# Kernel optimization log

Hardware: AMD Instinct MI355X
Metric: run time of the kernel (lower is better)

Reference implementation:

```python
import jax, jax.numpy as jnp
import numpy as np

# Constants from the torch module
S_DECAY = 0.95    # sentence_decay
P_DECAY = 0.99    # paragraph_decay
D_DECAY = 0.999   # document_decay
ALPHA = 0.1       # delta_update alpha for sentence/paragraph
DOC_ALPHA = 0.05  # delta_update alpha for document
BETA = 1.0
PARA_GROUP = 5    # sentences per paragraph
EPS = 1e-12       # F.normalize eps


def _normalize(x):
    # matches torch.nn.functional.normalize(x, dim=-1)
    return x / jnp.maximum(jnp.linalg.norm(x, axis=-1, keepdims=True), EPS)


def _delta_step(M, kn, v, alpha, beta):
    # M: [H, dk, dv]; kn: [dk] (already L2-normalized); v: [dv]
    # M_new = M @ (I - alpha * kn kn^T) + beta * kn v^T   (erase matrix is symmetric,
    # so the einsum 'hkv,hkj->hjv' form equals this rank-1 update -- no dk x dk matrix needed)
    kTM = jnp.einsum('k,hkv->hv', kn, M)                       # [H, dv]
    return M - alpha * kn[None, :, None] * kTM[:, None, :] \
             + beta * (kn[:, None] * v[None, :])[None, :, :]


def _scan_updates(M0, K, V, decay, alpha, beta):
    # Streaming delta-rule: per step, decay then erase/write.
    def step(M, kv):
        k, v = kv
        M = M * decay
        M = _delta_step(M, _normalize(k), v, alpha, beta)
        return M, None
    M, _ = jax.lax.scan(step, M0, (K, V))
    return M


def setup_inputs() -> dict:
    key = jax.random.key(0)
    ks = jax.random.split(key, 7)
    T, d_emb, d_k, d_v, H = 1000, 768, 256, 256, 8
    emb = jax.random.normal(ks[0], (T, d_emb), dtype=jnp.float32)
    q = jax.random.normal(ks[1], (d_k,), dtype=jnp.float32)
    W_k = jax.random.normal(ks[2], (d_emb, d_k), dtype=jnp.float32) * 0.02
    b_k = jax.random.normal(ks[3], (d_k,), dtype=jnp.float32) * 0.02
    W_v = jax.random.normal(ks[4], (d_emb, d_v), dtype=jnp.float32) * 0.02
    b_v = jax.random.normal(ks[5], (d_v,), dtype=jnp.float32) * 0.02
    M_sent0 = jnp.zeros((H, d_k, d_v), dtype=jnp.float32)
    M_para0 = jnp.zeros((H, d_k, d_v), dtype=jnp.float32)
    M_doc0 = jnp.zeros((H, d_k, d_v), dtype=jnp.float32)
    return {"emb": emb, "q": q, "W_k": W_k, "b_k": b_k, "W_v": W_v, "b_v": b_v,
            "M_sent0": M_sent0, "M_para0": M_para0, "M_doc0": M_doc0}


def reference(emb, q, W_k, b_k, W_v, b_v, M_sent0, M_para0, M_doc0):
    T, d_emb = emb.shape
    # Level 1: sentence memory -- one delta update per sentence embedding
    K = emb @ W_k + b_k            # [T, dk]
    V = emb @ W_v + b_v            # [T, dv]
    M_sent = _scan_updates(M_sent0, K, V, S_DECAY, ALPHA, BETA)
    # Level 2: paragraph memory -- mean of each group of 5 sentence embeddings
    para_emb = emb.reshape(T // PARA_GROUP, PARA_GROUP, d_emb).mean(axis=1)
    PK = para_emb @ W_k + b_k
    PV = para_emb @ W_v + b_v
    M_para = _scan_updates(M_para0, PK, PV, P_DECAY, ALPHA, BETA)
    # Level 3: document memory -- single update from paragraph-memory statistics
    doc_k = M_para.mean(axis=0).mean(axis=-1)   # [dk]
    doc_v = M_para.mean(axis=0).mean(axis=0)    # [dv]
    M_doc = M_doc0 * D_DECAY
    M_doc = _delta_step(M_doc, _normalize(doc_k), doc_v, DOC_ALPHA, BETA)
    # recall(q, level='all')
    qn = _normalize(q)
    def recall(M):
        return jnp.einsum('hkv,k->hv', M, qn).mean(axis=0)   # [dv]
    return 0.2 * recall(M_sent) + 0.3 * recall(M_para) + 0.5 * recall(M_doc)
```

## Files before the change

### kernel.cpp

```cpp
#include <hip/hip_runtime.h>
#include <hip/hip_bf16.h>

#define ALPHA   0.1f
#define S_DECAY 0.95f
#define P_DECAY 0.99f
#define D_EMB   768
#define DK      256

template<int ctrl, int row_mask>
__device__ __forceinline__ float dpp_add(float x) {
    int y = __builtin_amdgcn_update_dpp(0, __float_as_int(x), ctrl, row_mask, 0xF, true);
    return x + __int_as_float(y);
}

template<int N>
__device__ __forceinline__ void wave_allred_arr(float (&x)[N]) {
#pragma unroll
    for (int n = 0; n < N; ++n) x[n] = dpp_add<0xB1,  0xF>(x[n]);
#pragma unroll
    for (int n = 0; n < N; ++n) x[n] = dpp_add<0x4E,  0xF>(x[n]);
#pragma unroll
    for (int n = 0; n < N; ++n) x[n] = dpp_add<0x141, 0xF>(x[n]);
#pragma unroll
    for (int n = 0; n < N; ++n) x[n] = dpp_add<0x140, 0xF>(x[n]);
#pragma unroll
    for (int n = 0; n < N; ++n) x[n] = dpp_add<0x142, 0xA>(x[n]);
#pragma unroll
    for (int n = 0; n < N; ++n) x[n] = dpp_add<0x143, 0xC>(x[n]);
#pragma unroll
    for (int n = 0; n < N; ++n)
        x[n] = __int_as_float(__builtin_amdgcn_readlane(__float_as_int(x[n]), 63));
}

__device__ __forceinline__ float dot4v(const float4& a, const float4& b) {
    float t0 = a.x * b.x; t0 = fmaf(a.y, b.y, t0);
    float t1 = a.z * b.z; t1 = fmaf(a.w, b.w, t1);
    return t0 + t1;
}

__global__ __launch_bounds__(256) void prep_kernel(
    const float* __restrict__ emb,
    const float* __restrict__ Wk, const float* __restrict__ bk,
    const float* __restrict__ Wv, const float* __restrict__ bv,
    float* __restrict__ K, float* __restrict__ V, float* __restrict__ USrev,
    float* __restrict__ out, int T)
{
    const int tid = threadIdx.x;
    const int bid = blockIdx.x;
    const int NBLK = (T / 4) * 2;
    if (bid >= NBLK) {
        const int PADS = ((T + 63) / 64) * 64;
        for (int i = tid; i < (PADS - T) * DK; i += 256) USrev[(size_t)T * DK + i] = 0.f;
        out[tid] = 0.f;
        return;
    }
    const int mat = bid & 1;
    const int r0  = (bid >> 1) * 4;

    __shared__ float se[4][D_EMB];
    __shared__ float s_red[4][4];

    const float4* emb4 = reinterpret_cast<const float4*>(emb);
#pragma unroll
    for (int r = 0; r < 4; ++r) {
        if (tid < D_EMB / 4)
            reinterpret_cast<float4*>(se[r])[tid] = emb4[(size_t)(r0 + r) * (D_EMB / 4) + tid];
    }
    __syncthreads();

    const float* Wp = mat ? Wv : Wk;
    const float* bp = mat ? bv : bk;
    const int j = tid;

    float a0 = 0.f, a1 = 0.f, a2 = 0.f, a3 = 0.f;
    float c0 = Wp[j],        c1 = Wp[j + DK],     c2 = Wp[j + 2*DK], c3 = Wp[j + 3*DK];
    float p0 = Wp[j + 4*DK], p1 = Wp[j + 5*DK],   p2 = Wp[j + 6*DK], p3 = Wp[j + 7*DK];

    for (int d = 0; d < D_EMB; d += 4) {
        int dn = d + 8; if (dn >= D_EMB) dn = 0;
        const float* wn = Wp + (size_t)dn * DK + j;
        float n0 = wn[0], n1 = wn[DK], n2 = wn[2*DK], n3 = wn[3*DK];

        float4 e0 = *reinterpret_cast<const float4*>(&se[0][d]);
        float4 e1 = *reinterpret_cast<const float4*>(&se[1][d]);
        float4 e2 = *reinterpret_cast<const float4*>(&se[2][d]);
        float4 e3 = *reinterpret_cast<const float4*>(&se[3][d]);

        a0 = fmaf(e0.x, c0, a0); a0 = fmaf(e0.y, c1, a0);
        a0 = fmaf(e0.z, c2, a0); a0 = fmaf(e0.w, c3, a0);
        a1 = fmaf(e1.x, c0, a1); a1 = fmaf(e1.y, c1, a1);
        a1 = fmaf(e1.z, c2, a1); a1 = fmaf(e1.w, c3, a1);
        a2 = fmaf(e2.x, c0, a2); a2 = fmaf(e2.y, c1, a2);
        a2 = fmaf(e2.z, c2, a2); a2 = fmaf(e2.w, c3, a2);
        a3 = fmaf(e3.x, c0, a3); a3 = fmaf(e3.y, c1, a3);
        a3 = fmaf(e3.z, c2, a3); a3 = fmaf(e3.w, c3, a3);

        c0 = p0; c1 = p1; c2 = p2; c3 = p3;
        p0 = n0; p1 = n1; p2 = n2; p3 = n3;
    }

    float bj = bp[j];
    float o0 = a0 + bj, o1 = a1 + bj, o2 = a2 + bj, o3 = a3 + bj;
    float* dst = mat ? V : K;
    dst[(size_t)(r0 + 0) * DK + j] = o0;
    dst[(size_t)(r0 + 1) * DK + j] = o1;
    dst[(size_t)(r0 + 2) * DK + j] = o2;
    dst[(size_t)(r0 + 3) * DK + j] = o3;

    if (mat == 0) {
        const int wave = tid >> 6, l = tid & 63;
        float red[4] = { o0*o0, o1*o1, o2*o2, o3*o3 };
        wave_allred_arr(red);
        if (l == 0) {
            s_red[wave][0] = red[0]; s_red[wave][1] = red[1];
            s_red[wave][2] = red[2]; s_red[wave][3] = red[3];
        }
        __syncthreads();
        float t0 = s_red[0][0] + s_red[1][0] + s_red[2][0] + s_red[3][0];
        float t1 = s_red[0][1] + s_red[1][1] + s_red[2][1] + s_red[3][1];
        float t2 = s_red[0][2] + s_red[1][2] + s_red[2][2] + s_red[3][2];
        float t3 = s_red[0][3] + s_red[1][3] + s_red[2][3] + s_red[3][3];
        USrev[(size_t)(T - 1 - (r0 + 0)) * DK + j] = o0 * (1.0f / fmaxf(sqrtf(t0), 1e-12f));
        USrev[(size_t)(T - 1 - (r0 + 1)) * DK + j] = o1 * (1.0f / fmaxf(sqrtf(t1), 1e-12f));
        USrev[(size_t)(T - 1 - (r0 + 2)) * DK + j] = o2 * (1.0f / fmaxf(sqrtf(t2), 1e-12f));
        USrev[(size_t)(T - 1 - (r0 + 3)) * DK + j] = o3 * (1.0f / fmaxf(sqrtf(t3), 1e-12f));
    }
}

__global__ __launch_bounds__(256) void graminv_kernel(
    const float* __restrict__ K, const float* __restrict__ V,
    const float* __restrict__ USrev,
    float* __restrict__ UPrev, float* __restrict__ UPfwd,
    float* __restrict__ PV, float* __restrict__ SVv,
    float* __restrict__ AinvT, float* __restrict__ Wall,
    float* __restrict__ F1, float* __restrict__ biasF,
    int P, int NCS, int NCP)
{
    __shared__ float sU[64 * 257];
    __shared__ float sA[64 * 65];
    __shared__ float sX[64 * 65];
    __shared__ float s_sv[64];
    __shared__ float s_pd[64];
    __shared__ float4 s_f1[4];
    __shared__ float4 s_f1w[4][64];
    const int tid = threadIdx.x, wv = tid >> 6, l = tid & 63;
    const int bid = blockIdx.x;
    int type, m;
    if (bid < NCS)            { type = 0; m = bid; }
    else if (bid < NCS + NCP) { type = 1; m = bid - NCS; }
    else                      { type = 2; m = bid - NCS - NCP; }

    if (tid < 64) s_pd[tid] = powf(P_DECAY, (float)tid);

    float4 f1p = make_float4(0.f, 0.f, 0.f, 0.f);

    if (type == 0) {
        const float4* U4 = reinterpret_cast<const float4*>(USrev) + (size_t)m * 4096;
        for (int idx = tid; idx < 4096; idx += 256) {
            float4 t = U4[idx];
            int row = idx >> 6, c4 = (idx & 63) << 2;
            float* b = &sU[row * 257 + c4];
            b[0] = t.x; b[1] = t.y; b[2] = t.z; b[3] = t.w;
        }
    } else if (type == 1) {
        const float4* K4 = reinterpret_cast<const float4*>(K);
        for (int ii = 0; ii < 16; ++ii) {
            int i = wv * 16 + ii;
            int p = P - 1 - (64 * m + i);
            float4 u = make_float4(0.f, 0.f, 0.f, 0.f);
            if (p >= 0) {
                float4 pk = make_float4(0.f, 0.f, 0.f, 0.f);
#pragma unroll
                for (int s = 0; s < 5; ++s) {
                    float4 k4 = K4[(size_t)(5 * p + s) * 64 + l];
                    pk.x += k4.x; pk.y += k4.y; pk.z += k4.z; pk.w += k4.w;
                }
                pk.x *= 0.2f; pk.y *= 0.2f; pk.z *= 0.2f; pk.w *= 0.2f;
                float red[1] = { dot4v(pk, pk) };
                wave_allred_arr(red);
                float inv = 1.0f / fmaxf(sqrtf(red[0]), 1e-12f);
                u = make_float4(pk.x * inv, pk.y * inv, pk.z * inv, pk.w * inv);
            }
            float* b = &sU[i * 257 + 4 * l];
            b[0] = u.x; b[1] = u.y; b[2] = u.z; b[3] = u.w;
            reinterpret_cast<float4*>(UPrev)[(size_t)(64 * m + i) * 64 + l] = u;
        }
    } else {
        const float4* K4 = reinterpret_cast<const float4*>(K);
        const float4* V4 = reinterpret_cast<const float4*>(V);
        for (int ii = 0; ii < 16; ++ii) {
            int i = wv * 16 + ii;
            int p = 64 * m + i;
            float4 u = make_float4(0.f, 0.f, 0.f, 0.f);
            float sv = 0.f;
            if (p < P) {
                float4 pk = make_float4(0.f, 0.f, 0.f, 0.f);
                float4 pv = make_float4(0.f, 0.f, 0.f, 0.f);
#pragma unroll
                for (int s = 0; s < 5; ++s) {
                    float4 k4 = K4[(size_t)(5 * p + s) * 64 + l];
                    float4 v4 = V4[(size_t)(5 * p + s) * 64 + l];
                    pk.x += k4.x; pk.y += k4.y; pk.z += k4.z; pk.w += k4.w;
                    pv.x += v4.x; pv.y += v4.y; pv.z += v4.z; pv.w += v4.w;
                }
                pk.x *= 0.2f; pk.y *= 0.2f; pk.z *= 0.2f; pk.w *= 0.2f;
                pv.x *= 0.2f; pv.y *= 0.2f; pv.z *= 0.2f; pv.w *= 0.2f;
                reinterpret_cast<float4*>(PV)[(size_t)p * 64 + l] = pv;
                float red[2] = { dot4v(pk, pk), pv.x + pv.y + pv.z + pv.w };
                wave_allred_arr(red);
                float inv = 1.0f / fmaxf(sqrtf(red[0]), 1e-12f);
                u = make_float4(pk.x * inv, pk.y * inv, pk.z * inv, pk.w * inv);
                sv = red[1];
            }
            float* b = &sU[i * 257 + 4 * l];
            b[0] = u.x; b[1] = u.y; b[2] = u.z; b[3] = u.w;
            reinterpret_cast<float4*>(UPfwd)[(size_t)(64 * m + i) * 64 + l] = u;
            if (l == 0) { s_sv[i] = sv; SVv[64 * m + i] = sv; }
            float f = powf(P_DECAY, (float)(63 - i)) * sv;
            f1p.x = fmaf(f, u.x, f1p.x); f1p.y = fmaf(f, u.y, f1p.y);
            f1p.z = fmaf(f, u.z, f1p.z); f1p.w = fmaf(f, u.w, f1p.w);
        }
        s_f1w[wv][l] = f1p;
    }
    __syncthreads();

    if (type == 2 && wv == 0) {
        float4 a = s_f1w[0][l], b = s_f1w[1][l], c = s_f1w[2][l], d = s_f1w[3][l];
        float4 tot = make_float4(a.x+b.x+c.x+d.x, a.y+b.y+c.y+d.y,
                                 a.z+b.z+c.z+d.z, a.w+b.w+c.w+d.w);
        reinterpret_cast<float4*>(F1)[(size_t)m * 64 + l] = tot;
    }

    const int tr = tid & 15, tcg = tid >> 4;
    const int i0 = tr * 4, j0 = tcg * 4;
    {
        float g00=0,g01=0,g02=0,g03=0, g10=0,g11=0,g12=0,g13=0;
        float g20=0,g21=0,g22=0,g23=0, g30=0,g31=0,g32=0,g33=0;
        for (int k = 0; k < 256; ++k) {
            float aa0 = sU[(i0    ) * 257 + k];
            float aa1 = sU[(i0 + 1) * 257 + k];
            float aa2 = sU[(i0 + 2) * 257 + k];
            float aa3 = sU[(i0 + 3) * 257 + k];
            float bb0 = sU[(j0    ) * 257 + k];
            float bb1 = sU[(j0 + 1) * 257 + k];
            float bb2 = sU[(j0 + 2) * 257 + k];
            float bb3 = sU[(j0 + 3) * 257 + k];
            g00 = fmaf(aa0, bb0, g00); g01 = fmaf(aa0, bb1, g01);
            g02 = fmaf(aa0, bb2, g02); g03 = fmaf(aa0, bb3, g03);
            g10 = fmaf(aa1, bb0, g10); g11 = fmaf(aa1, bb1, g11);
            g12 = fmaf(aa1, bb2, g12); g13 = fmaf(aa1, bb3, g13);
            g20 = fmaf(aa2, bb0, g20); g21 = fmaf(aa2, bb1, g21);
            g22 = fmaf(aa2, bb2, g22); g23 = fmaf(aa2, bb3, g23);
            g30 = fmaf(aa3, bb0, g30); g31 = fmaf(aa3, bb1, g31);
            g32 = fmaf(aa3, bb2, g32); g33 = fmaf(aa3, bb3, g33);
        }
        float gt[4][4] = { {g00,g01,g02,g03}, {g10,g11,g12,g13},
                           {g20,g21,g22,g23}, {g30,g31,g32,g33} };
#pragma unroll
        for (int r = 0; r < 4; ++r)
#pragma unroll
            for (int c = 0; c < 4; ++c) {
                int gi = i0 + r, gj = j0 + c;
                float val = 0.f;
                if (gj < gi) {
                    val = ALPHA * gt[r][c];
                    if (type == 2) val *= s_pd[gi - gj];
                }
                sA[gi * 65 + gj] = val;
            }
    }
    __syncthreads();

    if (type == 2 && wv == 0) {
        float dotb = 0.f;
#pragma unroll
        for (int jj = 0; jj < 64; ++jj)
            dotb = fmaf(sA[l * 65 + jj], s_sv[jj], dotb);
        biasF[m * 64 + l] = dotb * (1.0f / ALPHA);
    }

    {
        const int base = wv * 16;
        float x[16];
#pragma unroll
        for (int r = 0; r < 16; ++r) x[r] = (base + r == l) ? 1.f : 0.f;
        for (int s = 0; s < 4; ++s) {
            if (wv == s) {
#pragma unroll
                for (int i = 1; i < 16; ++i)
#pragma unroll
                    for (int jj = 0; jj < 16; ++jj)
                        if (jj < i)
                            x[i] = fmaf(-sA[(base + i) * 65 + (base + jj)], x[jj], x[i]);
#pragma unroll
                for (int r = 0; r < 16; ++r) sX[(base + r) * 65 + l] = x[r];
            }
            __syncthreads();
            if (wv > s) {
#pragma unroll
                for (int i = 0; i < 16; ++i) {
                    float xi = sX[(s * 16 + i) * 65 + l];
#pragma unroll
                    for (int r = 0; r < 16; ++r)
                        x[r] = fmaf(-sA[(base + r) * 65 + (s * 16 + i)], xi, x[r]);
                }
            }
        }
    }
    __syncthreads();

    if (type != 2) {
        float* dstA = AinvT + (size_t)bid * 4096;
        for (int idx = tid; idx < 4096; idx += 256) {
            int jcol = idx >> 6, irow = idx & 63;
            dstA[idx] = sX[irow * 65 + jcol];
        }
    }

    {
        const int c0 = tcg * 16;
        float wacc[4][16];
#pragma unroll
        for (int r = 0; r < 4; ++r)
#pragma unroll
            for (int c = 0; c < 16; ++c) wacc[r][c] = 0.f;
        for (int i = 0; i < 64; ++i) {
            float x0 = sX[i * 65 + i0    ];
            float x1 = sX[i * 65 + i0 + 1];
            float x2 = sX[i * 65 + i0 + 2];
            float x3 = sX[i * 65 + i0 + 3];
            if (type == 2) {
                float f = s_pd[63 - i];
                x0 *= f; x1 *= f; x2 *= f; x3 *= f;
            }
#pragma unroll
            for (int c = 0; c < 16; ++c) {
                float u = sU[i * 257 + c0 + c];
                wacc[0][c] = fmaf(x0, u, wacc[0][c]);
                wacc[1][c] = fmaf(x1, u, wacc[1][c]);
                wacc[2][c] = fmaf(x2, u, wacc[2][c]);
                wacc[3][c] = fmaf(x3, u, wacc[3][c]);
            }
        }
        float* dstW = Wall + (size_t)bid * 16384;
#pragma unroll
        for (int r = 0; r < 4; ++r) {
#pragma unroll
            for (int c4 = 0; c4 < 4; ++c4) {
                float4 t = make_float4(wacc[r][c4*4], wacc[r][c4*4+1],
                                       wacc[r][c4*4+2], wacc[r][c4*4+3]);
                reinterpret_cast<float4*>(dstW)[((i0 + r) * 256 + c0 + c4*4) >> 2] = t;
            }
        }
    }
}

__global__ __launch_bounds__(512) void solve_kernel(
    const float* __restrict__ USrev, const float* __restrict__ UPrev,
    const float* __restrict__ UPfwd, const float* __restrict__ Wall,
    const float* __restrict__ F1, const float* __restrict__ biasF,
    const float* __restrict__ q,
    float* __restrict__ BS, float* __restrict__ BPB1, float* __restrict__ BPB2,
    float* __restrict__ gscal, int NCS, int NCP)
{
    __shared__ float4 s_part[2][8][64], s_part2[2][8][64];
    __shared__ float s_powd[65];
    const int tid = threadIdx.x, wave = tid >> 6, l = tid & 63;
    const int wb = wave * 8;
    if (tid <= 64) s_powd[tid] = powf(P_DECAY, (float)tid);

    float4 q4 = reinterpret_cast<const float4*>(q)[l];
    float qs[1] = { dot4v(q4, q4) };
    wave_allred_arr(qs);
    float qinv = 1.0f / fmaxf(sqrtf(qs[0]), 1e-12f);
    float4 qn = make_float4(q4.x * qinv, q4.y * qinv, q4.z * qinv, q4.w * qinv);
    __syncthreads();

    const float4* W4 = reinterpret_cast<const float4*>(Wall);

    if (blockIdx.x == 0) {
        float4 w1 = qn;
        const float4* U4 = reinterpret_cast<const float4*>(USrev);
        float4 curU[8];
#pragma unroll
        for (int r = 0; r < 8; ++r) curU[r] = U4[(size_t)(wb + r) * 64 + l];
        for (int m = 0; m < NCS; ++m) {
            float4 curW[8];
#pragma unroll
            for (int r = 0; r < 8; ++r)
                curW[r] = W4[(size_t)m * 4096 + (size_t)(wb + r) * 64 + l];
            float4 nxtU[8];
            if (m + 1 < NCS) {
#pragma unroll
                for (int r = 0; r < 8; ++r)
                    nxtU[r] = U4[(size_t)(m + 1) * 4096 + (size_t)(wb + r) * 64 + l];
            }
            float d[8];
#pragma unroll
            for (int r = 0; r < 8; ++r) d[r] = dot4v(curU[r], w1);
            wave_allred_arr(d);
            if (l == 0) {
#pragma unroll
                for (int r = 0; r < 8; ++r) BS[m * 64 + wb + r] = d[r];
            }
            float4 part = make_float4(0.f, 0.f, 0.f, 0.f);
#pragma unroll
            for (int r = 0; r < 8; ++r) {
                part.x = fmaf(d[r], curW[r].x, part.x);
                part.y = fmaf(d[r], curW[r].y, part.y);
                part.z = fmaf(d[r], curW[r].z, part.z);
                part.w = fmaf(d[r], curW[r].w, part.w);
            }
            s_part[m & 1][wave][l] = part;
            __syncthreads();
            float4 s = make_float4(0.f, 0.f, 0.f, 0.f);
#pragma unroll
            for (int w = 0; w < 8; ++w) {
                float4 p = s_part[m & 1][w][l];
                s.x += p.x; s.y += p.y; s.z += p.z; s.w += p.w;
            }
            w1.x = fmaf(-ALPHA, s.x, w1.x); w1.y = fmaf(-ALPHA, s.y, w1.y);
            w1.z = fmaf(-ALPHA, s.z, w1.z); w1.w = fmaf(-ALPHA, s.w, w1.w);
            if (m + 1 < NCS) {
#pragma unroll
                for (int r = 0; r < 8; ++r) curU[r] = nxtU[r];
            }
        }
    } else {
        {
            float4 w1 = qn;
            float4 w2 = make_float4(1.f, 1.f, 1.f, 1.f);
            const float4* U4 = reinterpret_cast<const float4*>(UPrev);
            float4 curU[8];
#pragma unroll
            for (int r = 0; r < 8; ++r) curU[r] = U4[(size_t)(wb + r) * 64 + l];
            for (int m = 0; m < NCP; ++m) {
                float4 curW[8];
#pragma unroll
                for (int r = 0; r < 8; ++r)
                    curW[r] = W4[(size_t)(NCS + m) * 4096 + (size_t)(wb + r) * 64 + l];
                float4 nxtU[8];
                if (m + 1 < NCP) {
#pragma unroll
                    for (int r = 0; r < 8; ++r)
                        nxtU[r] = U4[(size_t)(m + 1) * 4096 + (size_t)(wb + r) * 64 + l];
                }
                float d[16];
#pragma unroll
                for (int r = 0; r < 8; ++r) {
                    d[r]     = dot4v(curU[r], w1);
                    d[8 + r] = dot4v(curU[r], w2);
                }
                wave_allred_arr(d);
                if (l == 0) {
#pragma unroll
                    for (int r = 0; r < 8; ++r) {
                        BPB1[m * 64 + wb + r] = d[r];
                        BPB2[m * 64 + wb + r] = d[8 + r];
                    }
                }
                float4 p1 = make_float4(0.f,0.f,0.f,0.f), p2 = make_float4(0.f,0.f,0.f,0.f);
#pragma unroll
                for (int r = 0; r < 8; ++r) {
                    p1.x = fmaf(d[r], curW[r].x, p1.x);   p1.y = fmaf(d[r], curW[r].y, p1.y);
                    p1.z = fmaf(d[r], curW[r].z, p1.z);   p1.w = fmaf(d[r], curW[r].w, p1.w);
                    p2.x = fmaf(d[8+r], curW[r].x, p2.x); p2.y = fmaf(d[8+r], curW[r].y, p2.y);
                    p2.z = fmaf(d[8+r], curW[r].z, p2.z); p2.w = fmaf(d[8+r], curW[r].w, p2.w);
                }
                s_part[m & 1][wave][l] = p1; s_part2[m & 1][wave][l] = p2;
                __syncthreads();
                float4 s1 = make_float4(0.f,0.f,0.f,0.f), s2 = make_float4(0.f,0.f,0.f,0.f);
#pragma unroll
                for (int w = 0; w < 8; ++w) {
                    float4 a = s_part[m & 1][w][l];  float4 b = s_part2[m & 1][w][l];
                    s1.x += a.x; s1.y += a.y; s1.z += a.z; s1.w += a.w;
                    s2.x += b.x; s2.y += b.y; s2.z += b.z; s2.w += b.w;
                }
                w1.x = fmaf(-ALPHA, s1.x, w1.x); w1.y = fmaf(-ALPHA, s1.y, w1.y);
                w1.z = fmaf(-ALPHA, s1.z, w1.z); w1.w = fmaf(-ALPHA, s1.w, w1.w);
                w2.x = fmaf(-ALPHA, s2.x, w2.x); w2.y = fmaf(-ALPHA, s2.y, w2.y);
                w2.z = fmaf(-ALPHA, s2.z, w2.z); w2.w = fmaf(-ALPHA, s2.w, w2.w);
                if (m + 1 < NCP) {
#pragma unroll
                    for (int r = 0; r < 8; ++r) curU[r] = nxtU[r];
                }
            }
        }
        __syncthreads();
        float4 y = make_float4(0.f, 0.f, 0.f, 0.f);
        {
            const float4* U4 = reinterpret_cast<const float4*>(UPfwd);
            float4 curU[8];
#pragma unroll
            for (int r = 0; r < 8; ++r) curU[r] = U4[(size_t)(wb + r) * 64 + l];
            for (int m = 0; m < NCP; ++m) {
                float4 curW[8];
#pragma unroll
                for (int r = 0; r < 8; ++r)
                    curW[r] = W4[(size_t)(NCS + NCP + m) * 4096 + (size_t)(wb + r) * 64 + l];
                float biasr[8];
#pragma unroll
                for (int r = 0; r < 8; ++r) biasr[r] = biasF[m * 64 + wb + r];
                float4 f1 = reinterpret_cast<const float4*>(F1)[(size_t)m * 64 + l];
                float4 nxtU[8];
                if (m + 1 < NCP) {
#pragma unroll
                    for (int r = 0; r < 8; ++r)
                        nxtU[r] = U4[(size_t)(m + 1) * 4096 + (size_t)(wb + r) * 64 + l];
                }
                float d[8];
#pragma unroll
                for (int r = 0; r < 8; ++r) d[r] = dot4v(curU[r], y);
                wave_allred_arr(d);
#pragma unroll
                for (int r = 0; r < 8; ++r)
                    d[r] = fmaf(s_powd[wb + r + 1], d[r], biasr[r]);
                float4 part = make_float4(0.f, 0.f, 0.f, 0.f);
#pragma unroll
                for (int r = 0; r < 8; ++r) {
                    part.x = fmaf(d[r], curW[r].x, part.x);
                    part.y = fmaf(d[r], curW[r].y, part.y);
                    part.z = fmaf(d[r], curW[r].z, part.z);
                    part.w = fmaf(d[r], curW[r].w, part.w);
                }
                s_part[m & 1][wave][l] = part;
                __syncthreads();
                float4 s = make_float4(0.f, 0.f, 0.f, 0.f);
#pragma unroll
                for (int w = 0; w < 8; ++w) {
                    float4 p = s_part[m & 1][w][l];
                    s.x += p.x; s.y += p.y; s.z += p.z; s.w += p.w;
                }
                float d64 = s_powd[64];
                y.x = fmaf(d64, y.x, fmaf(-ALPHA, s.x, f1.x));
                y.y = fmaf(d64, y.y, fmaf(-ALPHA, s.y, f1.y));
                y.z = fmaf(d64, y.z, fmaf(-ALPHA, s.z, f1.z));
                y.w = fmaf(d64, y.w, fmaf(-ALPHA, s.w, f1.w));
                if (m + 1 < NCP) {
#pragma unroll
                    for (int r = 0; r < 8; ++r) curU[r] = nxtU[r];
                }
            }
        }
        float fin[2] = { dot4v(y, y), dot4v(qn, y) };
        wave_allred_arr(fin);
        if (tid == 0) gscal[0] = fin[1] / fmaxf(sqrtf(fin[0]), 2.56e-10f);
    }
}

__global__ __launch_bounds__(256) void accum_kernel(
    const float* __restrict__ V, const float* __restrict__ PV,
    const float* __restrict__ AinvT,
    const float* __restrict__ BS, const float* __restrict__ BPB1,
    const float* __restrict__ BPB2, const float* __restrict__ gscal,
    float* __restrict__ out, int T, int P, int NCS, int NCP)
{
    __shared__ float s_b[64], s_cp[4][64], wc[64];
    const int b = blockIdx.x, t = threadIdx.x;
    const float* src; const float* B; int i0, realN, chunk; float decay;
    if (b < NCS)            { src = V;  B = BS;   i0 = b * 64;               realN = T; decay = S_DECAY; chunk = b; }
    else if (b < NCS + NCP) { src = PV; B = BPB1; i0 = (b - NCS) * 64;       realN = P; decay = P_DECAY; chunk = b; }
    else                    { src = PV; B = BPB2; i0 = (b - NCS - NCP) * 64; realN = P; decay = P_DECAY; chunk = b - NCP; }
    if (t < 64) s_b[t] = B[(i0 & ~63) + t - i0 + i0];
    if (t < 64) s_b[t] = B[((b < NCS) ? b : (b < NCS + NCP ? b - NCS : b - NCS - NCP)) * 64 + t];
    __syncthreads();
    {
        const int part = t >> 6, k = t & 63;
        const float* Xc = AinvT + (size_t)chunk * 4096;
        float cp = 0.f;
#pragma unroll
        for (int jj = 0; jj < 16; ++jj) {
            int j = part * 16 + jj;
            cp = fmaf(Xc[j * 64 + k], s_b[j], cp);
        }
        s_cp[part][k] = cp;
    }
    __syncthreads();
    if (t < 64) {
        float c = s_cp[0][t] + s_cp[1][t] + s_cp[2][t] + s_cp[3][t];
        wc[t] = powf(decay, (float)(i0 + t)) * c;
    }
    __syncthreads();
    const int k = t;
    float acc = 0.f;
    for (int ii = 0; ii < 64; ++ii) {
        int i = i0 + ii;
        if (i < realN)
            acc = fmaf(wc[ii], src[(size_t)(realN - 1 - i) * DK + k], acc);
    }
    float wlev;
    if (b < NCS)            wlev = 0.2f;
    else if (b < NCS + NCP) wlev = 0.3f;
    else                    wlev = (0.5f / 256.0f) * gscal[0];
    atomicAdd(&out[k], wlev * acc);
}

extern "C" void kernel_launch(void* const* d_in, const int* in_sizes, int n_in,
                              void* d_out, int out_size, void* d_ws, size_t ws_size,
                              hipStream_t stream) {
    const float* emb = (const float*)d_in[0];
    const float* q   = (const float*)d_in[1];
    const float* Wk  = (const float*)d_in[2];
    const float* bk  = (const float*)d_in[3];
    const float* Wv  = (const float*)d_in[4];
    const float* bv  = (const float*)d_in[5];

    const int T = in_sizes[0] / D_EMB;
    const int P = T / 5;
    const int NCS  = (T + 63) / 64;
    const int NCP  = (P + 63) / 64;
    const int PADS = NCS * 64;
    const int PADP = NCP * 64;
    const int NCH  = NCS + 2 * NCP;

    float* ws    = (float*)d_ws;
    float* K     = ws;
    float* V     = K     + (size_t)T * DK;
    float* PV    = V     + (size_t)T * DK;
    float* USrev = PV    + (size_t)PADP * DK;
    float* UPrev = USrev + (size_t)PADS * DK;
    float* UPfwd = UPrev + (size_t)PADP * DK;
    float* SVv   = UPfwd + (size_t)PADP * DK;
    float* AinvT = SVv   + PADP;
    float* Wall  = AinvT + (size_t)NCH * 4096;
    float* F1    = Wall  + (size_t)NCH * 16384;
    float* biasF = F1    + (size_t)NCP * 256;
    float* BS    = biasF + PADP;
    float* BPB1  = BS    + PADS;
    float* BPB2  = BPB1  + PADP;
    float* gscal = BPB2  + PADP;

    prep_kernel<<<(T / 4) * 2 + 1, 256, 0, stream>>>(emb, Wk, bk, Wv, bv,
                                                     K, V, USrev, (float*)d_out, T);
    graminv_kernel<<<NCH, 256, 0, stream>>>(K, V, USrev, UPrev, UPfwd,
                                            PV, SVv, AinvT, Wall, F1, biasF, P, NCS, NCP);
    solve_kernel<<<2, 512, 0, stream>>>(USrev, UPrev, UPfwd, Wall, F1, biasF, q,
                                        BS, BPB1, BPB2, gscal, NCS, NCP);
    accum_kernel<<<NCH, 256, 0, stream>>>(V, PV, AinvT, BS, BPB1, BPB2, gscal,
                                          (float*)d_out, T, P, NCS, NCP);
}
```

Baseline: 198.4 us.

## Drop precomputed W matrices; apply inverse-then-U factored inside solve loop

The graminv kernel no longer builds and stores the per-chunk W = X·U products (64x256 per chunk) and only writes the transposed inverse. The sequential solve kernel instead applies X to the projected vector via a small cross-wave reduction, then broadcasts coefficients with readlane and multiplies by U, which it already loads. The Gram computation also uses float4 shared-memory reads with a padded stride and skips the upper-triangle tiles. This removes a large global write and read of W at the cost of an extra barrier and reduction per step in the latency-bound serial solve loop.

```diff
diff --git a/kernel.cpp b/kernel.cpp
--- a/kernel.cpp
+++ b/kernel.cpp
@@ -36,6 +36,10 @@
     float t0 = a.x * b.x; t0 = fmaf(a.y, b.y, t0);
     float t1 = a.z * b.z; t1 = fmaf(a.w, b.w, t1);
     return t0 + t1;
+}
+
+__device__ __forceinline__ float rl(float x, int lane) {
+    return __int_as_float(__builtin_amdgcn_readlane(__float_as_int(x), lane));
 }
 
 __global__ __launch_bounds__(256) void prep_kernel(
@@ -127,21 +131,20 @@
     }
 }
 
+#define SU_STRIDE 260
 __global__ __launch_bounds__(256) void graminv_kernel(
     const float* __restrict__ K, const float* __restrict__ V,
     const float* __restrict__ USrev,
     float* __restrict__ UPrev, float* __restrict__ UPfwd,
     float* __restrict__ PV, float* __restrict__ SVv,
-    float* __restrict__ AinvT, float* __restrict__ Wall,
-    float* __restrict__ F1, float* __restrict__ biasF,
+    float* __restrict__ AinvT, float* __restrict__ F1, float* __restrict__ biasF,
     int P, int NCS, int NCP)
 {
-    __shared__ float sU[64 * 257];
+    __shared__ float sU[64 * SU_STRIDE];
     __shared__ float sA[64 * 65];
     __shared__ float sX[64 * 65];
     __shared__ float s_sv[64];
     __shared__ float s_pd[64];
-    __shared__ float4 s_f1[4];
     __shared__ float4 s_f1w[4][64];
     const int tid = threadIdx.x, wv = tid >> 6, l = tid & 63;
     const int bid = blockIdx.x;
@@ -159,8 +162,7 @@
         for (int idx = tid; idx < 4096; idx += 256) {
             float4 t = U4[idx];
             int row = idx >> 6, c4 = (idx & 63) << 2;
-            float* b = &sU[row * 257 + c4];
-            b[0] = t.x; b[1] = t.y; b[2] = t.z; b[3] = t.w;
+            *reinterpret_cast<float4*>(&sU[row * SU_STRIDE + c4]) = t;
         }
     } else if (type == 1) {
         const float4* K4 = reinterpret_cast<const float4*>(K);
@@ -181,8 +183,7 @@
                 float inv = 1.0f / fmaxf(sqrtf(red[0]), 1e-12f);
                 u = make_float4(pk.x * inv, pk.y * inv, pk.z * inv, pk.w * inv);
             }
-            float* b = &sU[i * 257 + 4 * l];
-            b[0] = u.x; b[1] = u.y; b[2] = u.z; b[3] = u.w;
+            *reinterpret_cast<float4*>(&sU[i * SU_STRIDE + 4 * l]) = u;
             reinterpret_cast<float4*>(UPrev)[(size_t)(64 * m + i) * 64 + l] = u;
         }
     } else {
@@ -212,8 +213,7 @@
                 u = make_float4(pk.x * inv, pk.y * inv, pk.z * inv, pk.w * inv);
                 sv = red[1];
             }
-            float* b = &sU[i * 257 + 4 * l];
-            b[0] = u.x; b[1] = u.y; b[2] = u.z; b[3] = u.w;
+            *reinterpret_cast<float4*>(&sU[i * SU_STRIDE + 4 * l]) = u;
             reinterpret_cast<float4*>(UPfwd)[(size_t)(64 * m + i) * 64 + l] = u;
             if (l == 0) { s_sv[i] = sv; SVv[64 * m + i] = sv; }
             float f = powf(P_DECAY, (float)(63 - i)) * sv;
@@ -233,29 +233,30 @@
 
     const int tr = tid & 15, tcg = tid >> 4;
     const int i0 = tr * 4, j0 = tcg * 4;
-    {
-        float g00=0,g01=0,g02=0,g03=0, g10=0,g11=0,g12=0,g13=0;
-        float g20=0,g21=0,g22=0,g23=0, g30=0,g31=0,g32=0,g33=0;
-        for (int k = 0; k < 256; ++k) {
-            float aa0 = sU[(i0    ) * 257 + k];
-            float aa1 = sU[(i0 + 1) * 257 + k];
-            float aa2 = sU[(i0 + 2) * 257 + k];
-            float aa3 = sU[(i0 + 3) * 257 + k];
-            float bb0 = sU[(j0    ) * 257 + k];
-            float bb1 = sU[(j0 + 1) * 257 + k];
-            float bb2 = sU[(j0 + 2) * 257 + k];
-            float bb3 = sU[(j0 + 3) * 257 + k];
-            g00 = fmaf(aa0, bb0, g00); g01 = fmaf(aa0, bb1, g01);
-            g02 = fmaf(aa0, bb2, g02); g03 = fmaf(aa0, bb3, g03);
-            g10 = fmaf(aa1, bb0, g10); g11 = fmaf(aa1, bb1, g11);
-            g12 = fmaf(aa1, bb2, g12); g13 = fmaf(aa1, bb3, g13);
-            g20 = fmaf(aa2, bb0, g20); g21 = fmaf(aa2, bb1, g21);
-            g22 = fmaf(aa2, bb2, g22); g23 = fmaf(aa2, bb3, g23);
-            g30 = fmaf(aa3, bb0, g30); g31 = fmaf(aa3, bb1, g31);
-            g32 = fmaf(aa3, bb2, g32); g33 = fmaf(aa3, bb3, g33);
-        }
-        float gt[4][4] = { {g00,g01,g02,g03}, {g10,g11,g12,g13},
-                           {g20,g21,g22,g23}, {g30,g31,g32,g33} };
+    if (tcg <= tr) {
+        float g[4][4];
+#pragma unroll
+        for (int r = 0; r < 4; ++r)
+#pragma unroll
+            for (int c = 0; c < 4; ++c) g[r][c] = 0.f;
+        for (int k4 = 0; k4 < 64; ++k4) {
+            float4 A0 = *reinterpret_cast<const float4*>(&sU[(i0    ) * SU_STRIDE + 4*k4]);
+            float4 A1 = *reinterpret_cast<const float4*>(&sU[(i0 + 1) * SU_STRIDE + 4*k4]);
+            float4 A2 = *reinterpret_cast<const float4*>(&sU[(i0 + 2) * SU_STRIDE + 4*k4]);
+            float4 A3 = *reinterpret_cast<const float4*>(&sU[(i0 + 3) * SU_STRIDE + 4*k4]);
+            float4 B0 = *reinterpret_cast<const float4*>(&sU[(j0    ) * SU_STRIDE + 4*k4]);
+            float4 B1 = *reinterpret_cast<const float4*>(&sU[(j0 + 1) * SU_STRIDE + 4*k4]);
+            float4 B2 = *reinterpret_cast<const float4*>(&sU[(j0 + 2) * SU_STRIDE + 4*k4]);
+            float4 B3 = *reinterpret_cast<const float4*>(&sU[(j0 + 3) * SU_STRIDE + 4*k4]);
+            g[0][0] += dot4v(A0, B0); g[0][1] += dot4v(A0, B1);
+            g[0][2] += dot4v(A0, B2); g[0][3] += dot4v(A0, B3);
+            g[1][0] += dot4v(A1, B0); g[1][1] += dot4v(A1, B1);
+            g[1][2] += dot4v(A1, B2); g[1][3] += dot4v(A1, B3);
+            g[2][0] += dot4v(A2, B0); g[2][1] += dot4v(A2, B1);
+            g[2][2] += dot4v(A2, B2); g[2][3] += dot4v(A2, B3);
+            g[3][0] += dot4v(A3, B0); g[3][1] += dot4v(A3, B1);
+            g[3][2] += dot4v(A3, B2); g[3][3] += dot4v(A3, B3);
+        }
 #pragma unroll
         for (int r = 0; r < 4; ++r)
 #pragma unroll
@@ -263,11 +264,17 @@
                 int gi = i0 + r, gj = j0 + c;
                 float val = 0.f;
                 if (gj < gi) {
-                    val = ALPHA * gt[r][c];
+                    val = ALPHA * g[r][c];
                     if (type == 2) val *= s_pd[gi - gj];
                 }
                 sA[gi * 65 + gj] = val;
             }
+    } else {
+#pragma unroll
+        for (int r = 0; r < 4; ++r)
+#pragma unroll
+            for (int c = 0; c < 4; ++c)
+                sA[(i0 + r) * 65 + j0 + c] = 0.f;
     }
     __syncthreads();
 
@@ -309,61 +316,23 @@
     }
     __syncthreads();
 
-    if (type != 2) {
-        float* dstA = AinvT + (size_t)bid * 4096;
-        for (int idx = tid; idx < 4096; idx += 256) {
-            int jcol = idx >> 6, irow = idx & 63;
-            dstA[idx] = sX[irow * 65 + jcol];
-        }
-    }
-
-    {
-        const int c0 = tcg * 16;
-        float wacc[4][16];
-#pragma unroll
-        for (int r = 0; r < 4; ++r)
-#pragma unroll
-            for (int c = 0; c < 16; ++c) wacc[r][c] = 0.f;
-        for (int i = 0; i < 64; ++i) {
-            float x0 = sX[i * 65 + i0    ];
-            float x1 = sX[i * 65 + i0 + 1];
-            float x2 = sX[i * 65 + i0 + 2];
-            float x3 = sX[i * 65 + i0 + 3];
-            if (type == 2) {
-                float f = s_pd[63 - i];
-                x0 *= f; x1 *= f; x2 *= f; x3 *= f;
-            }
-#pragma unroll
-            for (int c = 0; c < 16; ++c) {
-                float u = sU[i * 257 + c0 + c];
-                wacc[0][c] = fmaf(x0, u, wacc[0][c]);
-                wacc[1][c] = fmaf(x1, u, wacc[1][c]);
-                wacc[2][c] = fmaf(x2, u, wacc[2][c]);
-                wacc[3][c] = fmaf(x3, u, wacc[3][c]);
-            }
-        }
-        float* dstW = Wall + (size_t)bid * 16384;
-#pragma unroll
-        for (int r = 0; r < 4; ++r) {
-#pragma unroll
-            for (int c4 = 0; c4 < 4; ++c4) {
-                float4 t = make_float4(wacc[r][c4*4], wacc[r][c4*4+1],
-                                       wacc[r][c4*4+2], wacc[r][c4*4+3]);
-                reinterpret_cast<float4*>(dstW)[((i0 + r) * 256 + c0 + c4*4) >> 2] = t;
-            }
-        }
+    float* dstA = AinvT + (size_t)bid * 4096;
+    for (int idx = tid; idx < 4096; idx += 256) {
+        int jcol = idx >> 6, irow = idx & 63;
+        dstA[idx] = sX[irow * 65 + jcol];
     }
 }
 
 __global__ __launch_bounds__(512) void solve_kernel(
     const float* __restrict__ USrev, const float* __restrict__ UPrev,
-    const float* __restrict__ UPfwd, const float* __restrict__ Wall,
+    const float* __restrict__ UPfwd, const float* __restrict__ AinvT,
     const float* __restrict__ F1, const float* __restrict__ biasF,
     const float* __restrict__ q,
     float* __restrict__ BS, float* __restrict__ BPB1, float* __restrict__ BPB2,
     float* __restrict__ gscal, int NCS, int NCP)
 {
-    __shared__ float4 s_part[2][8][64], s_part2[2][8][64];
+    __shared__ float s_cp[8][64], s_cp2[8][64];
+    __shared__ float4 s_part[8][64], s_part2[8][64];
     __shared__ float s_powd[65];
     const int tid = threadIdx.x, wave = tid >> 6, l = tid & 63;
     const int wb = wave * 8;
@@ -376,24 +345,23 @@
     float4 qn = make_float4(q4.x * qinv, q4.y * qinv, q4.z * qinv, q4.w * qinv);
     __syncthreads();
 
-    const float4* W4 = reinterpret_cast<const float4*>(Wall);
-
     if (blockIdx.x == 0) {
         float4 w1 = qn;
         const float4* U4 = reinterpret_cast<const float4*>(USrev);
-        float4 curU[8];
-#pragma unroll
-        for (int r = 0; r < 8; ++r) curU[r] = U4[(size_t)(wb + r) * 64 + l];
+        float4 curU[8]; float curX[8];
+#pragma unroll
+        for (int r = 0; r < 8; ++r) {
+            curU[r] = U4[(size_t)(wb + r) * 64 + l];
+            curX[r] = AinvT[(size_t)(wb + r) * 64 + l];
+        }
         for (int m = 0; m < NCS; ++m) {
-            float4 curW[8];
-#pragma unroll
-            for (int r = 0; r < 8; ++r)
-                curW[r] = W4[(size_t)m * 4096 + (size_t)(wb + r) * 64 + l];
-            float4 nxtU[8];
+            float4 nxtU[8]; float nxtX[8];
             if (m + 1 < NCS) {
 #pragma unroll
-                for (int r = 0; r < 8; ++r)
+                for (int r = 0; r < 8; ++r) {
                     nxtU[r] = U4[(size_t)(m + 1) * 4096 + (size_t)(wb + r) * 64 + l];
+                    nxtX[r] = AinvT[(size_t)(m + 1) * 4096 + (size_t)(wb + r) * 64 + l];
+                }
             }
             float d[8];
 #pragma unroll
@@ -403,27 +371,34 @@
 #pragma unroll
                 for (int r = 0; r < 8; ++r) BS[m * 64 + wb + r] = d[r];
             }
+            float cp = 0.f;
+#pragma unroll
+            for (int r = 0; r < 8; ++r) cp = fmaf(curX[r], d[r], cp);
+            s_cp[wave][l] = cp;
+            __syncthreads();
+            float cl = 0.f;
+#pragma unroll
+            for (int w = 0; w < 8; ++w) cl += s_cp[w][l];
             float4 part = make_float4(0.f, 0.f, 0.f, 0.f);
 #pragma unroll
             for (int r = 0; r < 8; ++r) {
-                part.x = fmaf(d[r], curW[r].x, part.x);
-                part.y = fmaf(d[r], curW[r].y, part.y);
-                part.z = fmaf(d[r], curW[r].z, part.z);
-                part.w = fmaf(d[r], curW[r].w, part.w);
-            }
-            s_part[m & 1][wave][l] = part;
+                float ci = rl(cl, wb + r);
+                part.x = fmaf(ci, curU[r].x, part.x); part.y = fmaf(ci, curU[r].y, part.y);
+                part.z = fmaf(ci, curU[r].z, part.z); part.w = fmaf(ci, curU[r].w, part.w);
+            }
+            s_part[wave][l] = part;
             __syncthreads();
             float4 s = make_float4(0.f, 0.f, 0.f, 0.f);
 #pragma unroll
             for (int w = 0; w < 8; ++w) {
-                float4 p = s_part[m & 1][w][l];
+                float4 p = s_part[w][l];
                 s.x += p.x; s.y += p.y; s.z += p.z; s.w += p.w;
             }
             w1.x = fmaf(-ALPHA, s.x, w1.x); w1.y = fmaf(-ALPHA, s.y, w1.y);
             w1.z = fmaf(-ALPHA, s.z, w1.z); w1.w = fmaf(-ALPHA, s.w, w1.w);
             if (m + 1 < NCS) {
 #pragma unroll
-                for (int r = 0; r < 8; ++r) curU[r] = nxtU[r];
+                for (int r = 0; r < 8; ++r) { curU[r] = nxtU[r]; curX[r] = nxtX[r]; }
             }
         }
     } else {
@@ -431,19 +406,20 @@
             float4 w1 = qn;
             float4 w2 = make_float4(1.f, 1.f, 1.f, 1.f);
             const float4* U4 = reinterpret_cast<const float4*>(UPrev);
-            float4 curU[8];
-#pragma unroll
-            for (int r = 0; r < 8; ++r) curU[r] = U4[(size_t)(wb + r) * 64 + l];
+            float4 curU[8]; float curX[8];
+#pragma unroll
+            for (int r = 0; r < 8; ++r) {
+                curU[r] = U4[(size_t)(wb + r) * 64 + l];
+                curX[r] = AinvT[(size_t)NCS * 4096 + (size_t)(wb + r) * 64 + l];
+            }
             for (int m = 0; m < NCP; ++m) {
-                float4 curW[8];
-#pragma unroll
-                for (int r = 0; r < 8; ++r)
-                    curW[r] = W4[(size_t)(NCS + m) * 4096 + (size_t)(wb + r) * 64 + l];
-                float4 nxtU[8];
+                float4 nxtU[8]; float nxtX[8];
                 if (m + 1 < NCP) {
 #pragma unroll
-                    for (int r = 0; r < 8; ++r)
+                    for (int r = 0; r < 8; ++r) {
                         nxtU[r] = U4[(size_t)(m + 1) * 4096 + (size_t)(wb + r) * 64 + l];
+                        nxtX[r] = AinvT[(size_t)(NCS + m + 1) * 4096 + (size_t)(wb + r) * 64 + l];
+                    }
                 }
                 float d[16];
 #pragma unroll
@@ -459,20 +435,32 @@
                         BPB2[m * 64 + wb + r] = d[8 + r];
                     }
                 }
+                float cp1 = 0.f, cp2 = 0.f;
+#pragma unroll
+                for (int r = 0; r < 8; ++r) {
+                    cp1 = fmaf(curX[r], d[r], cp1);
+                    cp2 = fmaf(curX[r], d[8 + r], cp2);
+                }
+                s_cp[wave][l] = cp1; s_cp2[wave][l] = cp2;
+                __syncthreads();
+                float cl1 = 0.f, cl2 = 0.f;
+#pragma unroll
+                for (int w = 0; w < 8; ++w) { cl1 += s_cp[w][l]; cl2 += s_cp2[w][l]; }
                 float4 p1 = make_float4(0.f,0.f,0.f,0.f), p2 = make_float4(0.f,0.f,0.f,0.f);
 #pragma unroll
                 for (int r = 0; r < 8; ++r) {
-                    p1.x = fmaf(d[r], curW[r].x, p1.x);   p1.y = fmaf(d[r], curW[r].y, p1.y);
-                    p1.z = fmaf(d[r], curW[r].z, p1.z);   p1.w = fmaf(d[r], curW[r].w, p1.w);
-                    p2.x = fmaf(d[8+r], curW[r].x, p2.x); p2.y = fmaf(d[8+r], curW[r].y, p2.y);
-                    p2.z = fmaf(d[8+r], curW[r].z, p2.z); p2.w = fmaf(d[8+r], curW[r].w, p2.w);
-                }
-                s_part[m & 1][wave][l] = p1; s_part2[m & 1][wave][l] = p2;
+                    float c1 = rl(cl1, wb + r), c2 = rl(cl2, wb + r);
+                    p1.x = fmaf(c1, curU[r].x, p1.x); p1.y = fmaf(c1, curU[r].y, p1.y);
+                    p1.z = fmaf(c1, curU[r].z, p1.z); p1.w = fmaf(c1, curU[r].w, p1.w);
+                    p2.x = fmaf(c2, curU[r].x, p2.x); p2.y = fmaf(c2, curU[r].y, p2.y);
+                    p2.z = fmaf(c2, curU[r].z, p2.z); p2.w = fmaf(c2, curU[r].w, p2.w);
+                }
+                s_part[wave][l] = p1; s_part2[wave][l] = p2;
                 __syncthreads();
                 float4 s1 = make_float4(0.f,0.f,0.f,0.f), s2 = make_float4(0.f,0.f,0.f,0.f);
 #pragma unroll
                 for (int w = 0; w < 8; ++w) {
-                    float4 a = s_part[m & 1][w][l];  float4 b = s_part2[m & 1][w][l];
+                    float4 a = s_part[w][l];  float4 b = s_part2[w][l];
                     s1.x += a.x; s1.y += a.y; s1.z += a.z; s1.w += a.w;
                     s2.x += b.x; s2.y += b.y; s2.z += b.z; s2.w += b.w;
                 }
@@ -482,7 +470,7 @@
                 w2.z = fmaf(-ALPHA, s2.z, w2.z); w2.w = fmaf(-ALPHA, s2.w, w2.w);
                 if (m + 1 < NCP) {
 #pragma unroll
-                    for (int r = 0; r < 8; ++r) curU[r] = nxtU[r];
+                    for (int r = 0; r < 8; ++r) { curU[r] = nxtU[r]; curX[r] = nxtX[r]; }
                 }
             }
         }
@@ -490,24 +478,25 @@
         float4 y = make_float4(0.f, 0.f, 0.f, 0.f);
         {
             const float4* U4 = reinterpret_cast<const float4*>(UPfwd);
-            float4 curU[8];
-#pragma unroll
-            for (int r = 0; r < 8; ++r) curU[r] = U4[(size_t)(wb + r) * 64 + l];
+            float4 curU[8]; float curX[8];
+#pragma unroll
+            for (int r = 0; r < 8; ++r) {
+                curU[r] = U4[(size_t)(wb + r) * 64 + l];
+                curX[r] = AinvT[(size_t)(NCS + NCP) * 4096 + (size_t)(wb + r) * 64 + l];
+            }
             for (int m = 0; m < NCP; ++m) {
-                float4 curW[8];
-#pragma unroll
-                for (int r = 0; r < 8; ++r)
-                    curW[r] = W4[(size_t)(NCS + NCP + m) * 4096 + (size_t)(wb + r) * 64 + l];
+                float4 nxtU[8]; float nxtX[8];
+                if (m + 1 < NCP) {
+#pragma unroll
+                    for (int r = 0; r < 8; ++r) {
+                        nxtU[r] = U4[(size_t)(m + 1) * 4096 + (size_t)(wb + r) * 64 + l];
+                        nxtX[r] = AinvT[(size_t)(NCS + NCP + m + 1) * 4096 + (size_t)(wb + r) * 64 + l];
+                    }
+                }
                 float biasr[8];
 #pragma unroll
                 for (int r = 0; r < 8; ++r) biasr[r] = biasF[m * 64 + wb + r];
                 float4 f1 = reinterpret_cast<const float4*>(F1)[(size_t)m * 64 + l];
-                float4 nxtU[8];
-                if (m + 1 < NCP) {
-#pragma unroll
-                    for (int r = 0; r < 8; ++r)
-                        nxtU[r] = U4[(size_t)(m + 1) * 4096 + (size_t)(wb + r) * 64 + l];
-                }
                 float d[8];
 #pragma unroll
                 for (int r = 0; r < 8; ++r) d[r] = dot4v(curU[r], y);
@@ -515,20 +504,27 @@
 #pragma unroll
                 for (int r = 0; r < 8; ++r)
                     d[r] = fmaf(s_powd[wb + r + 1], d[r], biasr[r]);
+                float cp = 0.f;
+#pragma unroll
+                for (int r = 0; r < 8; ++r) cp = fmaf(curX[r], d[r], cp);
+                s_cp[wave][l] = cp;
+                __syncthreads();
+                float cl = 0.f;
+#pragma unroll
+                for (int w = 0; w < 8; ++w) cl += s_cp[w][l];
                 float4 part = make_float4(0.f, 0.f, 0.f, 0.f);
 #pragma unroll
                 for (int r = 0; r < 8; ++r) {
-                    part.x = fmaf(d[r], curW[r].x, part.x);
-                    part.y = fmaf(d[r], curW[r].y, part.y);
-                    part.z = fmaf(d[r], curW[r].z, part.z);
-                    part.w = fmaf(d[r], curW[r].w, part.w);
-                }
-                s_part[m & 1][wave][l] = part;
+                    float ci = s_powd[63 - (wb + r)] * rl(cl, wb + r);
+                    part.x = fmaf(ci, curU[r].x, part.x); part.y = fmaf(ci, curU[r].y, part.y);
+                    part.z = fmaf(ci, curU[r].z, part.z); part.w = fmaf(ci, curU[r].w, part.w);
+                }
+                s_part[wave][l] = part;
                 __syncthreads();
                 float4 s = make_float4(0.f, 0.f, 0.f, 0.f);
 #pragma unroll
                 for (int w = 0; w < 8; ++w) {
-                    float4 p = s_part[m & 1][w][l];
+                    float4 p = s_part[w][l];
                     s.x += p.x; s.y += p.y; s.z += p.z; s.w += p.w;
                 }
                 float d64 = s_powd[64];
@@ -538,7 +534,7 @@
                 y.w = fmaf(d64, y.w, fmaf(-ALPHA, s.w, f1.w));
                 if (m + 1 < NCP) {
 #pragma unroll
-                    for (int r = 0; r < 8; ++r) curU[r] = nxtU[r];
+                    for (int r = 0; r < 8; ++r) { curU[r] = nxtU[r]; curX[r] = nxtX[r]; }
                 }
             }
         }
@@ -557,12 +553,12 @@
 {
     __shared__ float s_b[64], s_cp[4][64], wc[64];
     const int b = blockIdx.x, t = threadIdx.x;
-    const float* src; const float* B; int i0, realN, chunk; float decay;
-    if (b < NCS)            { src = V;  B = BS;   i0 = b * 64;               realN = T; decay = S_DECAY; chunk = b; }
-    else if (b < NCS + NCP) { src = PV; B = BPB1; i0 = (b - NCS) * 64;       realN = P; decay = P_DECAY; chunk = b; }
-    else                    { src = PV; B = BPB2; i0 = (b - NCS - NCP) * 64; realN = P; decay = P_DECAY; chunk = b - NCP; }
-    if (t < 64) s_b[t] = B[(i0 & ~63) + t - i0 + i0];
-    if (t < 64) s_b[t] = B[((b < NCS) ? b : (b < NCS + NCP ? b - NCS : b - NCS - NCP)) * 64 + t];
+    const float* src; const float* B; int i0, realN, chunk, ci; float decay;
+    if (b < NCS)            { src = V;  B = BS;   ci = b;             realN = T; decay = S_DECAY; chunk = b; }
+    else if (b < NCS + NCP) { src = PV; B = BPB1; ci = b - NCS;       realN = P; decay = P_DECAY; chunk = b; }
+    else                    { src = PV; B = BPB2; ci = b - NCS - NCP; realN = P; decay = P_DECAY; chunk = b - NCP; }
+    i0 = ci * 64;
+    if (t < 64) s_b[t] = B[ci * 64 + t];
     __syncthreads();
     {
         const int part = t >> 6, k = t & 63;
@@ -622,8 +618,7 @@
     float* UPfwd = UPrev + (size_t)PADP * DK;
     float* SVv   = UPfwd + (size_t)PADP * DK;
     float* AinvT = SVv   + PADP;
-    float* Wall  = AinvT + (size_t)NCH * 4096;
-    float* F1    = Wall  + (size_t)NCH * 16384;
+    float* F1    = AinvT + (size_t)NCH * 4096;
     float* biasF = F1    + (size_t)NCP * 256;
     float* BS    = biasF + PADP;
     float* BPB1  = BS    + PADS;
@@ -633,8 +628,8 @@
     prep_kernel<<<(T / 4) * 2 + 1, 256, 0, stream>>>(emb, Wk, bk, Wv, bv,
                                                      K, V, USrev, (float*)d_out, T);
     graminv_kernel<<<NCH, 256, 0, stream>>>(K, V, USrev, UPrev, UPfwd,
-                                            PV, SVv, AinvT, Wall, F1, biasF, P, NCS, NCP);
-    solve_kernel<<<2, 512, 0, stream>>>(USrev, UPrev, UPfwd, Wall, F1, biasF, q,
+                                            PV, SVv, AinvT, F1, biasF, P, NCS, NCP);
+    solve_kernel<<<2, 512, 0, stream>>>(USrev, UPrev, UPfwd, AinvT, F1, biasF, q,
                                         BS, BPB1, BPB2, gscal, NCS, NCP);
     accum_kernel<<<NCH, 256, 0, stream>>>(V, PV, AinvT, BS, BPB1, BPB2, gscal,
                                           (float*)d_out, T, P, NCS, NCP);
```

Measured after the change: 186.0 us. 6.3% less time.
